# Kernel optimization log

Measured on AMD Instinct MI355X. Metric: run time of the kernel, lower is better.

Reference implementation:

```python
import jax, jax.numpy as jnp
import numpy as np
from jax import lax

NUM_GROUPS = 16
EPS = 1e-5  # PyTorch GroupNorm default
POOL = 2
CLAMP_MIN, CLAMP_MAX = 0.0, 1.0


def setup_inputs() -> dict:
    key = jax.random.key(0)
    ks = jax.random.split(key, 6)
    B, Cin, H, W = 32, 64, 128, 128
    Cout, K = 128, 3
    return {
        "x": jax.random.normal(ks[0], (B, Cin, H, W), dtype=jnp.float32),
        "conv_w": jax.random.normal(ks[1], (Cout, Cin, K, K), dtype=jnp.float32),
        "conv_b": jax.random.normal(ks[2], (Cout,), dtype=jnp.float32),
        "gn_w": jax.random.normal(ks[3], (Cout,), dtype=jnp.float32),
        "gn_b": jax.random.normal(ks[4], (Cout,), dtype=jnp.float32),
        "scale": jax.random.normal(ks[5], (Cout, 1, 1), dtype=jnp.float32),
    }


def reference(x, conv_w, conv_b, gn_w, gn_b, scale):
    # Conv2d, stride 1, no padding (PyTorch default): [B,Cout,H-2,W-2]
    y = lax.conv_general_dilated(
        x, conv_w, window_strides=(1, 1), padding="VALID",
        dimension_numbers=("NCHW", "OIHW", "NCHW"))
    y = y + conv_b[None, :, None, None]

    # GroupNorm over (C/G, H, W) per sample and group
    B, C, H, W = y.shape
    yg = y.reshape(B, NUM_GROUPS, C // NUM_GROUPS, H, W)
    mean = jnp.mean(yg, axis=(2, 3, 4), keepdims=True)
    var = jnp.var(yg, axis=(2, 3, 4), keepdims=True)
    yn = ((yg - mean) * lax.rsqrt(var + EPS)).reshape(B, C, H, W)
    yn = yn * gn_w[None, :, None, None] + gn_b[None, :, None, None]

    # channel-wise scale (scale shape [C,1,1])
    yn = yn * scale[None, :, :, :]

    # MaxPool2d(kernel=2, stride=2)
    p = lax.reduce_window(yn, -jnp.inf, lax.max,
                          (1, 1, POOL, POOL), (1, 1, POOL, POOL), "VALID")

    # clamp
    return jnp.clip(p, CLAMP_MIN, CLAMP_MAX)
```

## Files before the change

### kernel.cpp

```cpp
#include <hip/hip_runtime.h>
#include <hip/hip_fp16.h>

#define CIN   64
#define COUT  128
#define HIN   128
#define WIN   128
#define HOUT  126
#define WOUT  126
#define HP    63
#define WP    63
#define NB    32
#define NG    16
#define EPS   1e-5f
#define KTOT  576
#define NTILE 252

#define XTROW (WIN * 64)
#define XTIMG (HIN * XTROW)

#define LROW  2176
#define LROWB 4352

typedef __attribute__((ext_vector_type(8))) _Float16 half8;
typedef __attribute__((ext_vector_type(4))) float f32x4;

#define GLOAD_LDS(gsrc, ldst)                                              \
    __builtin_amdgcn_global_load_lds(                                      \
        (const __attribute__((address_space(1))) void*)(gsrc),             \
        (__attribute__((address_space(3))) void*)(ldst), 16, 0, 0)

__global__ __launch_bounds__(256) void wprep_kernel(
    const float* __restrict__ cw, ushort* __restrict__ wt)
{
    int idx = blockIdx.x * 256 + threadIdx.x;
    if (idx >= COUT * KTOT) return;
    int co = idx / KTOT, k = idx - co * KTOT;
    int khw = k >> 6, ci = k & 63;
    float v = cw[(co * CIN + ci) * 9 + khw];
    wt[idx] = __half_as_ushort(__float2half(v));
}

__global__ __launch_bounds__(512) void xprep_kernel(
    const float* __restrict__ x, ushort* __restrict__ xt)
{
    const int tid = threadIdx.x;
    const int row = blockIdx.x & 127, b = blockIdx.x >> 7;
    const int cig = tid >> 6;
    const float* xb = x + (size_t)b * (CIN * HIN * WIN) + (size_t)row * WIN;
    ushort* ob = xt + (size_t)b * XTIMG + (size_t)row * XTROW;
#pragma unroll
    for (int ch = 0; ch < 2; ++ch) {
        int col = ch * 64 + (tid & 63);
        ushort v[8];
#pragma unroll
        for (int j = 0; j < 8; ++j)
            v[j] = __half_as_ushort(__float2half(
                xb[(size_t)(cig * 8 + j) * (HIN * WIN) + col]));
        uint4 pk;
        pk.x = (unsigned)v[0] | ((unsigned)v[1] << 16);
        pk.y = (unsigned)v[2] | ((unsigned)v[3] << 16);
        pk.z = (unsigned)v[4] | ((unsigned)v[5] << 16);
        pk.w = (unsigned)v[6] | ((unsigned)v[7] << 16);
        *(uint4*)(ob + col * 64 + ((cig ^ (col & 7)) * 8)) = pk;
    }
}

__global__ __launch_bounds__(256, 4) void conv_mfma_kernel(
    const ushort* __restrict__ xt, const ushort* __restrict__ wt,
    const float* __restrict__ cb, const float* __restrict__ gwv,
    const float* __restrict__ scv, float* __restrict__ m,
    float* __restrict__ partials)
{
    __shared__ ushort xs[4 * LROW];

    const int tid = threadIdx.x;
    const int bid = blockIdx.x;
    const int w   = (bid & 7) * 1008 + (bid >> 3);
    const int b   = w / 252;
    const int r   = w - b * 252;
    const int rp  = r >> 2;
    const int ct  = r & 3;
    const int r0x = rp * 2;

    const int l = tid & 63, wg = tid >> 6;
    const int l15 = l & 15, lhi = l >> 4;

    const ushort* xtb = xt + (size_t)b * XTIMG + (size_t)r0x * XTROW
                      + (size_t)(ct * 32) * 64;
#pragma unroll
    for (int t = 0; t < 5; ++t) {
        int idx = t * 256 + tid;
        if (idx < 1088) {
            int row = idx / 272;
            int within = idx - row * 272;
            GLOAD_LDS(xtb + (size_t)row * XTROW + within * 8, &xs[idx * 8]);
        }
    }
    __syncthreads();

    f32x4 acc[2][4];
#pragma unroll
    for (int mt = 0; mt < 2; ++mt)
#pragma unroll
        for (int nt = 0; nt < 4; ++nt)
            acc[mt][nt] = (f32x4){0.f, 0.f, 0.f, 0.f};

    const ushort* wb = wt + (size_t)(wg * 32 + l15) * KTOT + lhi * 8;
    const char* xsb = (const char*)xs;

#pragma unroll
    for (int khw = 0; khw < 9; ++khw) {
        const int kh = khw / 3, kw = khw - kh * 3;
        const int c7 = (l15 + kw) & 7;
#pragma unroll
        for (int cip = 0; cip < 2; ++cip) {
            half8 a0 = *(const half8*)(wb + khw * 64 + cip * 32);
            half8 a1 = *(const half8*)(wb + 16 * KTOT + khw * 64 + cip * 32);
            const int s = ((cip * 4 + lhi) ^ c7) * 16;
            half8 bv[4];
#pragma unroll
            for (int nt = 0; nt < 4; ++nt)
                bv[nt] = *(const half8*)(xsb + ((nt >> 1) + kh) * LROWB
                        + ((nt & 1) * 16 + kw + l15) * 128 + s);
#pragma unroll
            for (int nt = 0; nt < 4; ++nt) {
                acc[0][nt] = __builtin_amdgcn_mfma_f32_16x16x32_f16(
                    a0, bv[nt], acc[0][nt], 0, 0, 0);
                acc[1][nt] = __builtin_amdgcn_mfma_f32_16x16x32_f16(
                    a1, bv[nt], acc[1][nt], 0, 0, 0);
            }
        }
    }

#pragma unroll
    for (int mt = 0; mt < 2; ++mt) {
        float s1 = 0.f, s2 = 0.f;
#pragma unroll
        for (int r2 = 0; r2 < 4; ++r2) {
            int co = wg * 32 + mt * 16 + lhi * 4 + r2;
            float bias = cb[co];
            bool usemax = (gwv[co] * scv[co]) >= 0.f;
#pragma unroll
            for (int nc = 0; nc < 2; ++nc) {
                float v0 = acc[mt][nc][r2] + bias;
                float v1 = acc[mt][2 + nc][r2] + bias;
                int col = ct * 32 + nc * 16 + l15;
                if (col < WOUT) { s1 += v0 + v1; s2 += v0 * v0 + v1 * v1; }
                float a = usemax ? fmaxf(v0, v1) : fminf(v0, v1);
                float xo = __shfl_xor(a, 1);
                float wv = usemax ? fmaxf(a, xo) : fminf(a, xo);
                int wp = col >> 1;
                if (((l15 & 1) == 0) && wp < WP)
                    m[(((size_t)(b * COUT + co)) * HP + rp) * WP + wp] = wv;
            }
        }
#pragma unroll
        for (int d = 1; d < 16; d <<= 1) {
            s1 += __shfl_xor(s1, d);
            s2 += __shfl_xor(s2, d);
        }
        s1 += __shfl_xor(s1, 16);
        s2 += __shfl_xor(s2, 16);
        if (l15 == 0 && (lhi & 1) == 0) {
            int g = wg * 4 + mt * 2 + (lhi >> 1);
            size_t pidx = (((size_t)b * NG + g) * NTILE + (rp * 4 + ct)) * 2;
            partials[pidx + 0] = s1;
            partials[pidx + 1] = s2;
        }
    }
}

__global__ void stats_kernel(const float* __restrict__ partials,
                             float* __restrict__ stats)
{
    int t = blockIdx.x * blockDim.x + threadIdx.x;
    if (t >= NB * NG) return;
    float s1 = 0.f, s2 = 0.f;
    for (int j = 0; j < NTILE; ++j) {
        s1 += partials[((size_t)t * NTILE + j) * 2 + 0];
        s2 += partials[((size_t)t * NTILE + j) * 2 + 1];
    }
    const float N = 8.f * HOUT * WOUT;
    float mean = s1 / N;
    float var = s2 / N - mean * mean;
    stats[t * 2 + 0] = mean;
    stats[t * 2 + 1] = rsqrtf(var + EPS);
}

__global__ __launch_bounds__(256) void final_kernel(
    const float* __restrict__ m, const float* __restrict__ stats,
    const float* __restrict__ gw, const float* __restrict__ gb,
    const float* __restrict__ sc, float* __restrict__ out)
{
    int idx = blockIdx.x * 256 + threadIdx.x;
    if (idx >= NB * COUT * HP * WP) return;
    int t = idx / WP;
    t /= HP;
    int c = t % COUT;
    int b = t / COUT;
    int g = c >> 3;

    float mean = stats[(b * NG + g) * 2 + 0];
    float rstd = stats[(b * NG + g) * 2 + 1];
    float ga = rstd * gw[c] * sc[c];
    float gbb = (gb[c] - mean * rstd * gw[c]) * sc[c];

    float v = fmaf(m[idx], ga, gbb);
    out[idx] = fminf(fmaxf(v, 0.f), 1.f);
}

extern "C" void kernel_launch(void* const* d_in, const int* in_sizes, int n_in,
                              void* d_out, int out_size, void* d_ws, size_t ws_size,
                              hipStream_t stream)
{
    const float* x  = (const float*)d_in[0];
    const float* cw = (const float*)d_in[1];
    const float* cbias = (const float*)d_in[2];
    const float* gw = (const float*)d_in[3];
    const float* gb = (const float*)d_in[4];
    const float* sc = (const float*)d_in[5];
    float* out = (float*)d_out;

    const size_t MSZ = (size_t)NB * COUT * HP * WP;
    float* m        = (float*)d_ws;
    float* partials = m + MSZ;
    float* stats    = partials + (size_t)NB * NG * NTILE * 2;
    ushort* wt      = (ushort*)(stats + 1024);
    ushort* xtb     = wt + (size_t)COUT * KTOT;

    hipLaunchKernelGGL(wprep_kernel, dim3((COUT * KTOT + 255) / 256), dim3(256),
                       0, stream, cw, wt);

    hipLaunchKernelGGL(xprep_kernel, dim3(NB * HIN), dim3(512), 0, stream,
                       x, xtb);

    hipLaunchKernelGGL(conv_mfma_kernel, dim3(8064), dim3(256), 0, stream,
                       xtb, wt, cbias, gw, sc, m, partials);

    hipLaunchKernelGGL(stats_kernel, dim3(2), dim3(256), 0, stream,
                       partials, stats);

    int total = NB * COUT * HP * WP;
    hipLaunchKernelGGL(final_kernel, dim3((total + 255) / 256), dim3(256), 0, stream,
                       m, stats, gw, gb, sc, out);
}
```

Measured before the change: 247.9 us.

## Make conv blocks persistent over four pooled rows with double-buffered LDS staging

Each conv block now handles four consecutive pooled output rows instead of one, with the grid cut from 8064 to 2048 blocks. Block entry loads all weight fragments into registers once. Input rows are staged into a double-buffered LDS tile with async global-to-LDS loads so the next tile's fetch overlaps the current tile's MFMAs. GroupNorm partial sums are accumulated across the tiles, which shrinks the partials array. The extra registers (held weights) and double LDS lower the occupancy target to 2 blocks per SIMD-level launch bound, and fewer blocks may leave the GPU less evenly loaded.

```diff
diff --git a/kernel.cpp b/kernel.cpp
--- a/kernel.cpp
+++ b/kernel.cpp
@@ -13,13 +13,14 @@
 #define NG    16
 #define EPS   1e-5f
 #define KTOT  576
-#define NTILE 252
+#define NTILE 64
 
 #define XTROW (WIN * 64)
 #define XTIMG (HIN * XTROW)
 
 #define LROW  2176
 #define LROWB 4352
+#define LTILE (4 * LROW)
 
 typedef __attribute__((ext_vector_type(8))) _Float16 half8;
 typedef __attribute__((ext_vector_type(4))) float f32x4;
@@ -65,95 +66,129 @@
     }
 }
 
-__global__ __launch_bounds__(256, 4) void conv_mfma_kernel(
+__global__ __launch_bounds__(256, 2) void conv_mfma_kernel(
     const ushort* __restrict__ xt, const ushort* __restrict__ wt,
     const float* __restrict__ cb, const float* __restrict__ gwv,
     const float* __restrict__ scv, float* __restrict__ m,
     float* __restrict__ partials)
 {
-    __shared__ ushort xs[4 * LROW];
+    __shared__ ushort xs[2 * LTILE];
 
     const int tid = threadIdx.x;
     const int bid = blockIdx.x;
-    const int w   = (bid & 7) * 1008 + (bid >> 3);
-    const int b   = w / 252;
-    const int r   = w - b * 252;
-    const int rp  = r >> 2;
+    const int w   = (bid & 7) * 256 + (bid >> 3);
+    const int b   = w >> 6;
+    const int r   = w & 63;
+    const int rg  = r >> 2;
     const int ct  = r & 3;
-    const int r0x = rp * 2;
+    const int NT  = (rg == 15) ? 3 : 4;
 
     const int l = tid & 63, wg = tid >> 6;
     const int l15 = l & 15, lhi = l >> 4;
 
-    const ushort* xtb = xt + (size_t)b * XTIMG + (size_t)r0x * XTROW
-                      + (size_t)(ct * 32) * 64;
-#pragma unroll
-    for (int t = 0; t < 5; ++t) {
-        int idx = t * 256 + tid;
-        if (idx < 1088) {
-            int row = idx / 272;
-            int within = idx - row * 272;
-            GLOAD_LDS(xtb + (size_t)row * XTROW + within * 8, &xs[idx * 8]);
-        }
-    }
+    const ushort* xtbase = xt + (size_t)b * XTIMG + (size_t)(ct * 32) * 64;
+
+#define STAGE(t, bi)                                                       \
+    {                                                                      \
+        const ushort* src = xtbase + (size_t)(rg * 8 + 2 * (t)) * XTROW;   \
+        _Pragma("unroll")                                                  \
+        for (int tt = 0; tt < 5; ++tt) {                                   \
+            int idx = tt * 256 + tid;                                      \
+            if (idx < 1088) {                                              \
+                int row = idx / 272;                                       \
+                int within = idx - row * 272;                              \
+                GLOAD_LDS(src + (size_t)row * XTROW + within * 8,          \
+                          &xs[(bi) * LTILE + idx * 8]);                    \
+            }                                                              \
+        }                                                                  \
+    }
+
+    STAGE(0, 0);
+
+    const ushort* wb = wt + (size_t)(wg * 32 + l15) * KTOT + lhi * 8;
+    half8 wfa[2][9][2];
+#pragma unroll
+    for (int mt = 0; mt < 2; ++mt)
+#pragma unroll
+        for (int khw = 0; khw < 9; ++khw)
+#pragma unroll
+            for (int cip = 0; cip < 2; ++cip)
+                wfa[mt][khw][cip] = *(const half8*)(wb + mt * 16 * KTOT
+                                     + khw * 64 + cip * 32);
     __syncthreads();
 
-    f32x4 acc[2][4];
-#pragma unroll
-    for (int mt = 0; mt < 2; ++mt)
-#pragma unroll
-        for (int nt = 0; nt < 4; ++nt)
-            acc[mt][nt] = (f32x4){0.f, 0.f, 0.f, 0.f};
-
-    const ushort* wb = wt + (size_t)(wg * 32 + l15) * KTOT + lhi * 8;
-    const char* xsb = (const char*)xs;
-
-#pragma unroll
-    for (int khw = 0; khw < 9; ++khw) {
-        const int kh = khw / 3, kw = khw - kh * 3;
-        const int c7 = (l15 + kw) & 7;
-#pragma unroll
-        for (int cip = 0; cip < 2; ++cip) {
-            half8 a0 = *(const half8*)(wb + khw * 64 + cip * 32);
-            half8 a1 = *(const half8*)(wb + 16 * KTOT + khw * 64 + cip * 32);
-            const int s = ((cip * 4 + lhi) ^ c7) * 16;
-            half8 bv[4];
+    float s1acc[2] = {0.f, 0.f}, s2acc[2] = {0.f, 0.f};
+    const bool okc0 = (ct * 32 + 0 * 16 + l15) < WOUT;
+    const bool okc1 = (ct * 32 + 1 * 16 + l15) < WOUT;
+
+    for (int t = 0; t < NT; ++t) {
+        const int bi = t & 1;
+        if (t + 1 < NT) STAGE(t + 1, (t + 1) & 1);
+
+        f32x4 acc[2][4];
+#pragma unroll
+        for (int mt = 0; mt < 2; ++mt)
 #pragma unroll
             for (int nt = 0; nt < 4; ++nt)
-                bv[nt] = *(const half8*)(xsb + ((nt >> 1) + kh) * LROWB
-                        + ((nt & 1) * 16 + kw + l15) * 128 + s);
-#pragma unroll
-            for (int nt = 0; nt < 4; ++nt) {
-                acc[0][nt] = __builtin_amdgcn_mfma_f32_16x16x32_f16(
-                    a0, bv[nt], acc[0][nt], 0, 0, 0);
-                acc[1][nt] = __builtin_amdgcn_mfma_f32_16x16x32_f16(
-                    a1, bv[nt], acc[1][nt], 0, 0, 0);
+                acc[mt][nt] = (f32x4){0.f, 0.f, 0.f, 0.f};
+
+        const char* xc = (const char*)&xs[bi * LTILE];
+#pragma unroll
+        for (int khw = 0; khw < 9; ++khw) {
+            const int kh = khw / 3, kw = khw - kh * 3;
+            const int c7 = (l15 + kw) & 7;
+#pragma unroll
+            for (int cip = 0; cip < 2; ++cip) {
+                const int s = ((cip * 4 + lhi) ^ c7) * 16;
+                half8 bv[4];
+#pragma unroll
+                for (int nt = 0; nt < 4; ++nt)
+                    bv[nt] = *(const half8*)(xc + ((nt >> 1) + kh) * LROWB
+                            + ((nt & 1) * 16 + kw + l15) * 128 + s);
+#pragma unroll
+                for (int nt = 0; nt < 4; ++nt) {
+                    acc[0][nt] = __builtin_amdgcn_mfma_f32_16x16x32_f16(
+                        wfa[0][khw][cip], bv[nt], acc[0][nt], 0, 0, 0);
+                    acc[1][nt] = __builtin_amdgcn_mfma_f32_16x16x32_f16(
+                        wfa[1][khw][cip], bv[nt], acc[1][nt], 0, 0, 0);
+                }
             }
         }
-    }
+        __syncthreads();
+
+        const int rp = rg * 4 + t;
+#pragma unroll
+        for (int mt = 0; mt < 2; ++mt) {
+#pragma unroll
+            for (int r2 = 0; r2 < 4; ++r2) {
+                int co = wg * 32 + mt * 16 + lhi * 4 + r2;
+                float bias = cb[co];
+                bool usemax = (gwv[co] * scv[co]) >= 0.f;
+#pragma unroll
+                for (int nc = 0; nc < 2; ++nc) {
+                    float v0 = acc[mt][nc][r2] + bias;
+                    float v1 = acc[mt][2 + nc][r2] + bias;
+                    bool okc = nc ? okc1 : okc0;
+                    if (okc) {
+                        s1acc[mt] += v0 + v1;
+                        s2acc[mt] += v0 * v0 + v1 * v1;
+                    }
+                    float a = usemax ? fmaxf(v0, v1) : fminf(v0, v1);
+                    float xo = __shfl_xor(a, 1);
+                    float wv = usemax ? fmaxf(a, xo) : fminf(a, xo);
+                    int col = ct * 32 + nc * 16 + l15;
+                    int wp = col >> 1;
+                    if (((l15 & 1) == 0) && wp < WP)
+                        m[(((size_t)(b * COUT + co)) * HP + rp) * WP + wp] = wv;
+                }
+            }
+        }
+    }
+#undef STAGE
 
 #pragma unroll
     for (int mt = 0; mt < 2; ++mt) {
-        float s1 = 0.f, s2 = 0.f;
-#pragma unroll
-        for (int r2 = 0; r2 < 4; ++r2) {
-            int co = wg * 32 + mt * 16 + lhi * 4 + r2;
-            float bias = cb[co];
-            bool usemax = (gwv[co] * scv[co]) >= 0.f;
-#pragma unroll
-            for (int nc = 0; nc < 2; ++nc) {
-                float v0 = acc[mt][nc][r2] + bias;
-                float v1 = acc[mt][2 + nc][r2] + bias;
-                int col = ct * 32 + nc * 16 + l15;
-                if (col < WOUT) { s1 += v0 + v1; s2 += v0 * v0 + v1 * v1; }
-                float a = usemax ? fmaxf(v0, v1) : fminf(v0, v1);
-                float xo = __shfl_xor(a, 1);
-                float wv = usemax ? fmaxf(a, xo) : fminf(a, xo);
-                int wp = col >> 1;
-                if (((l15 & 1) == 0) && wp < WP)
-                    m[(((size_t)(b * COUT + co)) * HP + rp) * WP + wp] = wv;
-            }
-        }
+        float s1 = s1acc[mt], s2 = s2acc[mt];
 #pragma unroll
         for (int d = 1; d < 16; d <<= 1) {
             s1 += __shfl_xor(s1, d);
@@ -163,7 +198,7 @@
         s2 += __shfl_xor(s2, 16);
         if (l15 == 0 && (lhi & 1) == 0) {
             int g = wg * 4 + mt * 2 + (lhi >> 1);
-            size_t pidx = (((size_t)b * NG + g) * NTILE + (rp * 4 + ct)) * 2;
+            size_t pidx = (((size_t)b * NG + g) * NTILE + (rg * 4 + ct)) * 2;
             partials[pidx + 0] = s1;
             partials[pidx + 1] = s2;
         }
@@ -234,7 +269,7 @@
     hipLaunchKernelGGL(xprep_kernel, dim3(NB * HIN), dim3(512), 0, stream,
                        x, xtb);
 
-    hipLaunchKernelGGL(conv_mfma_kernel, dim3(8064), dim3(256), 0, stream,
+    hipLaunchKernelGGL(conv_mfma_kernel, dim3(2048), dim3(256), 0, stream,
                        xtb, wt, cbias, gw, sc, m, partials);
 
     hipLaunchKernelGGL(stats_kernel, dim3(2), dim3(256), 0, stream,
```

After: 268.1 us. 8.1% more time.

## Read conv input directly from global memory instead of LDS staging; parallelize stats

Applied to the files above, without the earlier changes.

The conv kernel no longer stages the input tile into shared memory with global_load_lds and a barrier. Each lane now reads its B-operand vectors straight from the channel-last fp16 buffer, relying on L1/L2 to serve the reuse, and the XOR swizzle is dropped from the input transpose. The stats reduction also changes from one thread per group with a serial loop to one wavefront per group with a shuffle reduction. This removes the LDS footprint and the barrier, which may raise occupancy, but it risks more global and cache traffic because the four waves of a block re-read the same input.

```diff
diff --git a/kernel.cpp b/kernel.cpp
--- a/kernel.cpp
+++ b/kernel.cpp
@@ -18,16 +18,8 @@
 #define XTROW (WIN * 64)
 #define XTIMG (HIN * XTROW)
 
-#define LROW  2176
-#define LROWB 4352
-
 typedef __attribute__((ext_vector_type(8))) _Float16 half8;
 typedef __attribute__((ext_vector_type(4))) float f32x4;
-
-#define GLOAD_LDS(gsrc, ldst)                                              \
-    __builtin_amdgcn_global_load_lds(                                      \
-        (const __attribute__((address_space(1))) void*)(gsrc),             \
-        (__attribute__((address_space(3))) void*)(ldst), 16, 0, 0)
 
 __global__ __launch_bounds__(256) void wprep_kernel(
     const float* __restrict__ cw, ushort* __restrict__ wt)
@@ -61,7 +53,7 @@
         pk.y = (unsigned)v[2] | ((unsigned)v[3] << 16);
         pk.z = (unsigned)v[4] | ((unsigned)v[5] << 16);
         pk.w = (unsigned)v[6] | ((unsigned)v[7] << 16);
-        *(uint4*)(ob + col * 64 + ((cig ^ (col & 7)) * 8)) = pk;
+        *(uint4*)(ob + col * 64 + cig * 8) = pk;
     }
 }
 
@@ -71,8 +63,6 @@
     const float* __restrict__ scv, float* __restrict__ m,
     float* __restrict__ partials)
 {
-    __shared__ ushort xs[4 * LROW];
-
     const int tid = threadIdx.x;
     const int bid = blockIdx.x;
     const int w   = (bid & 7) * 1008 + (bid >> 3);
@@ -85,19 +75,6 @@
     const int l = tid & 63, wg = tid >> 6;
     const int l15 = l & 15, lhi = l >> 4;
 
-    const ushort* xtb = xt + (size_t)b * XTIMG + (size_t)r0x * XTROW
-                      + (size_t)(ct * 32) * 64;
-#pragma unroll
-    for (int t = 0; t < 5; ++t) {
-        int idx = t * 256 + tid;
-        if (idx < 1088) {
-            int row = idx / 272;
-            int within = idx - row * 272;
-            GLOAD_LDS(xtb + (size_t)row * XTROW + within * 8, &xs[idx * 8]);
-        }
-    }
-    __syncthreads();
-
     f32x4 acc[2][4];
 #pragma unroll
     for (int mt = 0; mt < 2; ++mt)
@@ -105,23 +82,23 @@
         for (int nt = 0; nt < 4; ++nt)
             acc[mt][nt] = (f32x4){0.f, 0.f, 0.f, 0.f};
 
+    const ushort* xlane = xt + (size_t)b * XTIMG + (size_t)r0x * XTROW
+                        + (size_t)(ct * 32 + l15) * 64 + lhi * 8;
     const ushort* wb = wt + (size_t)(wg * 32 + l15) * KTOT + lhi * 8;
-    const char* xsb = (const char*)xs;
 
 #pragma unroll
     for (int khw = 0; khw < 9; ++khw) {
         const int kh = khw / 3, kw = khw - kh * 3;
-        const int c7 = (l15 + kw) & 7;
 #pragma unroll
         for (int cip = 0; cip < 2; ++cip) {
             half8 a0 = *(const half8*)(wb + khw * 64 + cip * 32);
             half8 a1 = *(const half8*)(wb + 16 * KTOT + khw * 64 + cip * 32);
-            const int s = ((cip * 4 + lhi) ^ c7) * 16;
             half8 bv[4];
 #pragma unroll
             for (int nt = 0; nt < 4; ++nt)
-                bv[nt] = *(const half8*)(xsb + ((nt >> 1) + kh) * LROWB
-                        + ((nt & 1) * 16 + kw + l15) * 128 + s);
+                bv[nt] = *(const half8*)(xlane
+                        + (size_t)((nt >> 1) + kh) * XTROW
+                        + ((nt & 1) * 16 + kw) * 64 + cip * 32);
 #pragma unroll
             for (int nt = 0; nt < 4; ++nt) {
                 acc[0][nt] = __builtin_amdgcn_mfma_f32_16x16x32_f16(
@@ -170,21 +147,28 @@
     }
 }
 
-__global__ void stats_kernel(const float* __restrict__ partials,
-                             float* __restrict__ stats)
-{
-    int t = blockIdx.x * blockDim.x + threadIdx.x;
-    if (t >= NB * NG) return;
+__global__ __launch_bounds__(64) void stats_kernel(
+    const float* __restrict__ partials, float* __restrict__ stats)
+{
+    int t = blockIdx.x;
+    int lane = threadIdx.x;
     float s1 = 0.f, s2 = 0.f;
-    for (int j = 0; j < NTILE; ++j) {
+    for (int j = lane; j < NTILE; j += 64) {
         s1 += partials[((size_t)t * NTILE + j) * 2 + 0];
         s2 += partials[((size_t)t * NTILE + j) * 2 + 1];
     }
-    const float N = 8.f * HOUT * WOUT;
-    float mean = s1 / N;
-    float var = s2 / N - mean * mean;
-    stats[t * 2 + 0] = mean;
-    stats[t * 2 + 1] = rsqrtf(var + EPS);
+#pragma unroll
+    for (int d = 1; d < 64; d <<= 1) {
+        s1 += __shfl_xor(s1, d);
+        s2 += __shfl_xor(s2, d);
+    }
+    if (lane == 0) {
+        const float N = 8.f * HOUT * WOUT;
+        float mean = s1 / N;
+        float var = s2 / N - mean * mean;
+        stats[t * 2 + 0] = mean;
+        stats[t * 2 + 1] = rsqrtf(var + EPS);
+    }
 }
 
 __global__ __launch_bounds__(256) void final_kernel(
@@ -237,7 +221,7 @@
     hipLaunchKernelGGL(conv_mfma_kernel, dim3(8064), dim3(256), 0, stream,
                        xtb, wt, cbias, gw, sc, m, partials);
 
-    hipLaunchKernelGGL(stats_kernel, dim3(2), dim3(256), 0, stream,
+    hipLaunchKernelGGL(stats_kernel, dim3(NB * NG), dim3(64), 0, stream,
                        partials, stats);
 
     int total = NB * COUT * HP * WP;
```

Measured after the change: 397.2 us. 1.6x slower.
